# Optimization experiments

Measured on AMD Instinct MI355X. Metric: run time of the kernel, lower is better.

The kernel has to match this reference:

```python
import jax, jax.numpy as jnp
import numpy as np

KE_KCAL = 332.0636  # Coulomb constant, kcal/mol * Angstrom / e^2
R_CUT = 5.0
R_ON = R_CUT / 4.0
R_OFF = 3.0 * R_CUT / 4.0
B, A, F = 32, 1024, 128  # molecules, atoms per molecule, feature dim
MAX_Z = 86


def silu(x):
    return x * jax.nn.sigmoid(x)


def res_mlp(x, W1, W2, Wout):
    # Residual (two pre-activation linears) -> activation -> Linear, no biases
    h = silu(x) @ W1
    h = silu(h) @ W2
    return silu(x + h) @ Wout


def f_switch(r):
    # smooth switching function built from sigma(x)=exp(-1/x) for x>0 else 0
    arg = (r - R_ON) / (R_OFF - R_ON)
    def sigma(x):
        xs = jnp.where(x > 0, x, 1.0)
        return jnp.where(x > 0, jnp.exp(-1.0 / xs), 0.0)
    num = sigma(1.0 - arg)
    return num / (num + sigma(arg))


def setup_inputs() -> dict:
    key = jax.random.key(0)
    ks = jax.random.split(key, 16)
    box = 22.0  # ~liquid density box for 1024 atoms (Angstrom)
    s = 1.0 / np.sqrt(F)
    return {
        'e_z': jax.random.normal(ks[0], (B * A, F), jnp.float32) * 0.1,
        'charge': jax.random.normal(ks[1], (B,), jnp.float32),
        'xyz': jax.random.uniform(ks[2], (B, A, 3), jnp.float32) * box,
        'W_lin': jax.random.normal(ks[3], (F, F), jnp.float32) * s,
        'b_lin': jnp.zeros((F,), jnp.float32),
        'k_plus': jax.random.normal(ks[4], (F,), jnp.float32) * s,
        'k_minus': jax.random.normal(ks[5], (F,), jnp.float32) * s,
        'v_plus': jax.random.normal(ks[6], (F,), jnp.float32) * s,
        'v_minus': jax.random.normal(ks[7], (F,), jnp.float32) * s,
        'Wr1': jax.random.normal(ks[8], (F, F), jnp.float32) * s,
        'Wr2': jax.random.normal(ks[9], (F, F), jnp.float32) * s,
        'Wout': jax.random.normal(ks[10], (F, F), jnp.float32) * s,
        'w_e': jax.random.normal(ks[11], (F,), jnp.float32) * s,
        'q_z_table': jax.random.normal(ks[12], (MAX_Z,), jnp.float32) * 0.01,
        'z': jax.random.randint(ks[13], (B * A,), 1, MAX_Z, jnp.int32),
    }


def reference(e_z, charge, xyz, W_lin, b_lin, k_plus, k_minus, v_plus, v_minus,
              Wr1, Wr2, Wout, w_e, q_z_table, z):
    # ---- ElectronicEmbedding (per-molecule loop vectorized over B) ----
    q = (e_z @ W_lin + b_lin).reshape(B, A, F)
    pos = (charge >= 0)[:, None]                       # [B,1]
    k = jnp.where(pos, k_plus[None, :], k_minus[None, :])   # [B,F]
    v = jnp.where(pos, v_plus[None, :], v_minus[None, :])   # [B,F]
    arg = jnp.einsum('baf,bf->ba', q, k) / np.sqrt(F)
    num = jax.nn.softplus(arg)                         # log(1+exp)
    a = charge[:, None] * num / num.sum(axis=1, keepdims=True)  # [B,A]
    av = a[:, :, None] * v[:, None, :]                 # [B,A,F]
    e_psi = res_mlp(av.reshape(B * A, F), Wr1, Wr2, Wout)
    f = e_z + e_psi                                    # atom features [N,F]

    # ---- Electrostatics.get_charge (charge-conserving correction) ----
    pred_q = (f @ w_e + q_z_table[z]).reshape(B, A)
    corr = (charge - pred_q.sum(axis=1)) / A
    q_atom = pred_q + corr[:, None]                    # [B,A]

    # ---- Electrostatics.get_en: O(A^2) pairwise switched Coulomb ----
    diff = xyz[:, :, None, :] - xyz[:, None, :, :]     # [B,A,A,3]
    r2 = jnp.sum(diff * diff, axis=-1)                 # [B,A,A]
    mask = jnp.triu(jnp.ones((A, A), bool), k=1)       # pairs j > i (r>0)
    r = jnp.sqrt(jnp.where(mask, r2, 1.0))
    fs = f_switch(r)
    coul = fs / jnp.sqrt(r * r + 1.0) + (1.0 - fs) / r
    pair_e = q_atom[:, :, None] * q_atom[:, None, :] * coul
    energy = KE_KCAL * jnp.sum(jnp.where(mask, pair_e, 0.0), axis=(1, 2))  # [B]
    return energy
```

## Files before the change

### kernel.cpp

```cpp
#include <hip/hip_runtime.h>
#include <math.h>

#define B_MOL 32
#define A_AT  1024
#define NF    128
#define N_AT  (B_MOL * A_AT)

#define WS_K2P     0
#define WS_K2M     128
#define WS_WOUT    256
#define WS_C       384
#define WS_NUMSUM  512
#define WS_PREDSUM 544
#define WS_NUM     1024
#define WS_EZWE    (WS_NUM + N_AT)
#define WS_PRED    (WS_EZWE + N_AT)
#define WS_SIDX    (WS_PRED + N_AT)
#define WS_SPOS    (WS_SIDX + N_AT)
#define WS_W1F     (WS_SPOS + 4 * N_AT)
#define WS_W2F     (WS_W1F + 8192)

typedef short short8 __attribute__((ext_vector_type(8)));
typedef float floatx4 __attribute__((ext_vector_type(4)));

__device__ __forceinline__ float fast_rcp(float x) { return __builtin_amdgcn_rcpf(x); }
__device__ __forceinline__ float fast_rsq(float x) { return __builtin_amdgcn_rsqf(x); }
__device__ __forceinline__ float silu_f(float x) { return x * fast_rcp(1.f + __expf(-x)); }

__device__ __forceinline__ short f2bf(float x) {
  unsigned u = __float_as_uint(x);
  u += 0x7fffu + ((u >> 16) & 1u);
  return (short)(u >> 16);
}

__device__ __forceinline__ float wave_sum(float v) {
#pragma unroll
  for (int o = 32; o > 0; o >>= 1) v += __shfl_xor(v, o, 64);
  return v;
}

__global__ __launch_bounds__(256) void pre_kernel(const float* __restrict__ W_lin,
                                                  const float* __restrict__ b_lin,
                                                  const float* __restrict__ k_plus,
                                                  const float* __restrict__ k_minus,
                                                  const float* __restrict__ Wout,
                                                  const float* __restrict__ w_e,
                                                  const float* __restrict__ Wr1,
                                                  const float* __restrict__ Wr2,
                                                  float* __restrict__ ws,
                                                  float* __restrict__ out) {
  int tid = threadIdx.x;
  if (blockIdx.x < 2) {
    const float* W = (blockIdx.x == 0) ? Wr1 : Wr2;
    short* dst = (short*)(ws + ((blockIdx.x == 0) ? WS_W1F : WS_W2F));
#pragma unroll
    for (int it = 0; it < 8; it++) {
      int idx = it * 256 + tid;
      int fi = idx >> 6, lane = idx & 63;
      int nt = fi >> 2, ks = fi & 3;
      int q = lane >> 4, n15 = lane & 15;
      int k0 = ks * 32 + q * 8;
      int col = nt * 16 + n15;
#pragma unroll
      for (int j = 0; j < 8; j++)
        dst[fi * 512 + lane * 8 + j] = f2bf(W[(k0 + j) * NF + col]);
    }
  } else {
    if (tid < 128) {
      float sp = 0.f, sm = 0.f;
      for (int f = 0; f < NF; f++) {
        float wl = W_lin[tid * NF + f];
        sp = fmaf(wl, k_plus[f], sp);
        sm = fmaf(wl, k_minus[f], sm);
      }
      ws[WS_K2P + tid] = sp;
      ws[WS_K2M + tid] = sm;
      if (tid < 2) {
        const float* kk = (tid == 0) ? k_plus : k_minus;
        float c = 0.f;
        for (int f = 0; f < NF; f++) c = fmaf(b_lin[f], kk[f], c);
        ws[WS_C + tid] = c;
      }
    } else {
      int g = tid - 128;
      float sw = 0.f;
      for (int f = 0; f < NF; f++) sw = fmaf(Wout[g * NF + f], w_e[f], sw);
      ws[WS_WOUT + g] = sw;
      if (g < 64) ws[WS_NUMSUM + g] = 0.f;
      if (g < 32) out[g] = 0.f;
    }
  }
}

__global__ __launch_bounds__(256) void sort_kernel(const float* __restrict__ xyz,
                                                   float* __restrict__ ws) {
  int mol = blockIdx.x, tid = threadIdx.x;
  __shared__ int hist[64], start[64];
  if (tid < 64) hist[tid] = 0;
  __syncthreads();
  float px[4], py[4], pz[4];
  int cell[4];
#pragma unroll
  for (int r = 0; r < 4; r++) {
    int j = tid + r * 256;
    const float* p = xyz + (size_t)(mol * A_AT + j) * 3;
    px[r] = p[0]; py[r] = p[1]; pz[r] = p[2];
    int cx = min(3, max(0, (int)(px[r] * (4.f / 22.f))));
    int cy = min(3, max(0, (int)(py[r] * (4.f / 22.f))));
    int cz = min(3, max(0, (int)(pz[r] * (4.f / 22.f))));
    cell[r] = cx * 16 + cy * 4 + cz;
    atomicAdd(&hist[cell[r]], 1);
  }
  __syncthreads();
  if (tid == 0) {
    int s = 0;
    for (int c = 0; c < 64; c++) { start[c] = s; s += hist[c]; }
  }
  __syncthreads();
  float4* spos = (float4*)(ws + WS_SPOS);
  int* sidx = (int*)ws + WS_SIDX;
#pragma unroll
  for (int r = 0; r < 4; r++) {
    int j = tid + r * 256;
    int off = atomicAdd(&start[cell[r]], 1);
    int g = mol * A_AT + off;
    spos[g] = make_float4(px[r], py[r], pz[r], 0.f);
    sidx[g] = j;
  }
}

__global__ __launch_bounds__(256) void attn_kernel(const float* __restrict__ e_z,
                                                   const float* __restrict__ charge,
                                                   const float* __restrict__ w_e,
                                                   float* __restrict__ ws) {
  int tid = threadIdx.x;
  int t = blockIdx.x * 256 + tid;
  int n = t >> 2;
  int part = t & 3;
  int mol = blockIdx.x >> 4;
  __shared__ float k2[NF], wesh[NF];
  float ch = charge[mol];
  if (tid < 128) {
    const float* k2src = ws + (ch >= 0.f ? WS_K2P : WS_K2M);
    k2[tid] = k2src[tid];
    wesh[tid] = w_e[tid];
  }
  float cc = ws[WS_C + (ch >= 0.f ? 0 : 1)];
  __syncthreads();
  const float4* row = (const float4*)(e_z + (size_t)n * NF + part * 32);
  float dk = 0.f, dw = 0.f;
#pragma unroll 8
  for (int i = 0; i < 8; i++) {
    float4 v = row[i];
    int b = part * 32 + i * 4;
    dk = fmaf(v.x, k2[b+0], dk); dk = fmaf(v.y, k2[b+1], dk);
    dk = fmaf(v.z, k2[b+2], dk); dk = fmaf(v.w, k2[b+3], dk);
    dw = fmaf(v.x, wesh[b+0], dw); dw = fmaf(v.y, wesh[b+1], dw);
    dw = fmaf(v.z, wesh[b+2], dw); dw = fmaf(v.w, wesh[b+3], dw);
  }
  dk += __shfl_xor(dk, 1, 64); dk += __shfl_xor(dk, 2, 64);
  dw += __shfl_xor(dw, 1, 64); dw += __shfl_xor(dw, 2, 64);
  float num = 0.f;
  if (part == 0) {
    float arg = (dk + cc) * 0.08838834764831845f;
    num = fmaxf(arg, 0.f) + log1pf(__expf(-fabsf(arg)));
    ws[WS_NUM + n] = num;
    ws[WS_EZWE + n] = dw;
  }
  float s = wave_sum(num);
  if ((tid & 63) == 0) atomicAdd(&ws[WS_NUMSUM + mol], s);
}

__global__ __launch_bounds__(256) void mlp_kernel(const float* __restrict__ charge,
                                                  const float* __restrict__ v_plus,
                                                  const float* __restrict__ v_minus,
                                                  const int* __restrict__ z,
                                                  const float* __restrict__ qz_table,
                                                  float* __restrict__ ws) {
  int base = blockIdx.x * 64;
  int mol = base >> 10;
  int tid = threadIdx.x;
  int w = tid >> 6;
  int lane = tid & 63;
  int q = lane >> 4, l15 = lane & 15;

  __shared__ short wf[16384];
  __shared__ short a2s[4 * 16 * 136];
  __shared__ float vsh[NF], wout_sh[NF], awsh[64], pred_sh[64];

  float ch = charge[mol];
  if (tid < 128) {
    vsh[tid] = (ch >= 0.f) ? v_plus[tid] : v_minus[tid];
    wout_sh[tid] = ws[WS_WOUT + tid];
  }
  if (tid < 64) awsh[tid] = ch * ws[WS_NUM + base + tid] / ws[WS_NUMSUM + mol];

  {
    const float4* src = (const float4*)(ws + WS_W1F);
    float4* dst = (float4*)wf;
#pragma unroll
    for (int r = 0; r < 8; r++) dst[tid + r * 256] = src[tid + r * 256];
  }
  __syncthreads();

  float aw_m = awsh[w * 16 + l15];
  floatx4 acc1[8];
#pragma unroll
  for (int nt = 0; nt < 8; nt++) acc1[nt] = (floatx4)(0.f);

#pragma unroll
  for (int ks = 0; ks < 4; ks++) {
    float4 va = *(const float4*)&vsh[ks * 32 + q * 8];
    float4 vb = *(const float4*)&vsh[ks * 32 + q * 8 + 4];
    short8 af;
    af[0] = f2bf(silu_f(aw_m * va.x)); af[1] = f2bf(silu_f(aw_m * va.y));
    af[2] = f2bf(silu_f(aw_m * va.z)); af[3] = f2bf(silu_f(aw_m * va.w));
    af[4] = f2bf(silu_f(aw_m * vb.x)); af[5] = f2bf(silu_f(aw_m * vb.y));
    af[6] = f2bf(silu_f(aw_m * vb.z)); af[7] = f2bf(silu_f(aw_m * vb.w));
#pragma unroll
    for (int nt = 0; nt < 8; nt++) {
      short8 bf = *(const short8*)&wf[(nt * 4 + ks) * 512 + lane * 8];
      acc1[nt] = __builtin_amdgcn_mfma_f32_16x16x32_bf16(af, bf, acc1[nt], 0, 0, 0);
    }
  }

#pragma unroll
  for (int nt = 0; nt < 8; nt++) {
    int f = nt * 16 + l15;
#pragma unroll
    for (int r = 0; r < 4; r++)
      a2s[w * 2176 + (q * 4 + r) * 136 + f] = f2bf(silu_f(acc1[nt][r]));
  }
  __syncthreads();
  {
    const float4* src = (const float4*)(ws + WS_W2F);
    float4* dst = (float4*)wf;
#pragma unroll
    for (int r = 0; r < 8; r++) dst[tid + r * 256] = src[tid + r * 256];
  }
  __syncthreads();

  floatx4 acc2[8];
#pragma unroll
  for (int nt = 0; nt < 8; nt++) acc2[nt] = (floatx4)(0.f);

#pragma unroll
  for (int ks = 0; ks < 4; ks++) {
    short8 af = *(const short8*)&a2s[w * 2176 + l15 * 136 + ks * 32 + q * 8];
#pragma unroll
    for (int nt = 0; nt < 8; nt++) {
      short8 bf = *(const short8*)&wf[(nt * 4 + ks) * 512 + lane * 8];
      acc2[nt] = __builtin_amdgcn_mfma_f32_16x16x32_bf16(af, bf, acc2[nt], 0, 0, 0);
    }
  }

  float awq[4], part[4];
#pragma unroll
  for (int r = 0; r < 4; r++) {
    awq[r] = awsh[w * 16 + q * 4 + r];
    part[r] = 0.f;
  }
#pragma unroll
  for (int nt = 0; nt < 8; nt++) {
    int f = nt * 16 + l15;
    float vv = vsh[f], ww = wout_sh[f];
#pragma unroll
    for (int r = 0; r < 4; r++) {
      float s = silu_f(fmaf(awq[r], vv, acc2[nt][r]));
      part[r] = fmaf(s, ww, part[r]);
    }
  }
#pragma unroll
  for (int r = 0; r < 4; r++) {
#pragma unroll
    for (int o = 1; o < 16; o <<= 1) part[r] += __shfl_xor(part[r], o, 64);
  }
  if (l15 == 0) {
#pragma unroll
    for (int r = 0; r < 4; r++) {
      int m = w * 16 + q * 4 + r;
      int n = base + m;
      float pred = part[r] + ws[WS_EZWE + n] + qz_table[z[n]];
      ws[WS_PRED + n] = pred;
      pred_sh[m] = pred;
    }
  }
  __syncthreads();
  if (tid < 64) {
    float s = wave_sum(pred_sh[tid]);
    if (tid == 0) atomicAdd(&ws[WS_PREDSUM + mol], s);
  }
}

__global__ __launch_bounds__(512) void pair_kernel(const float* __restrict__ xyz,
                                                   const float* __restrict__ charge,
                                                   float* __restrict__ ws,
                                                   float* __restrict__ out) {
  int bx = blockIdx.x;
  int mol = bx >> 4;
  int sub = bx & 15;
  int tid = threadIdx.x;
  __shared__ float4 posq[1024];
  __shared__ float wred[8];
  const float4* spos = (const float4*)(ws + WS_SPOS);
  const int* sidx = (const int*)ws + WS_SIDX;
  float corr = (charge[mol] - ws[WS_PREDSUM + mol]) * (1.f / 1024.f);
  for (int j = tid; j < 1024; j += 512) {
    float4 p = spos[mol * 1024 + j];
    p.w = ws[WS_PRED + mol * 1024 + sidx[mol * 1024 + j]] + corr;
    posq[j] = p;
  }
  __syncthreads();
  int i = sub * 64 + (tid & 63);
  int jq = tid >> 6;
  float4 me = posq[i];
  float e = 0.f;
  int j0 = jq * 128;
#pragma unroll 2
  for (int j = j0; j < j0 + 128; j++) {
    float4 p = posq[j];
    float dx = me.x - p.x, dy = me.y - p.y, dz = me.z - p.z;
    float r2 = fmaf(dx, dx, fmaf(dy, dy, dz * dz));
    bool self = (j == i);
    if (self) r2 = 1.0e8f;
    float qj = self ? 0.f : p.w;
    float inv_r = fast_rsq(r2);
    e = fmaf(qj, inv_r, e);
    if (__any(r2 < 14.0625f)) {
      float r = r2 * inv_r;
      float arg = (r - 1.25f) * 0.4f;
      float argc = fminf(fmaxf(arg, 1e-6f), 1.f - 1e-6f);
      float t = fast_rcp(argc) - fast_rcp(1.f - argc);
      float fs = fast_rcp(1.f + __expf(-t));
      float delta = fs * (fast_rsq(r2 + 1.f) - inv_r);
      e = fmaf(qj, delta, e);
    }
  }
  e *= me.w;
  float s = wave_sum(e);
  if ((tid & 63) == 0) wred[tid >> 6] = s;
  __syncthreads();
  if (tid == 0) {
    float tot = 0.f;
#pragma unroll
    for (int k = 0; k < 8; k++) tot += wred[k];
    atomicAdd(&out[mol], 166.0318f * tot);
  }
}

extern "C" void kernel_launch(void* const* d_in, const int* in_sizes, int n_in,
                              void* d_out, int out_size, void* d_ws, size_t ws_size,
                              hipStream_t stream) {
  const float* e_z     = (const float*)d_in[0];
  const float* charge  = (const float*)d_in[1];
  const float* xyz     = (const float*)d_in[2];
  const float* W_lin   = (const float*)d_in[3];
  const float* b_lin   = (const float*)d_in[4];
  const float* k_plus  = (const float*)d_in[5];
  const float* k_minus = (const float*)d_in[6];
  const float* v_plus  = (const float*)d_in[7];
  const float* v_minus = (const float*)d_in[8];
  const float* Wr1     = (const float*)d_in[9];
  const float* Wr2     = (const float*)d_in[10];
  const float* Wout    = (const float*)d_in[11];
  const float* w_e     = (const float*)d_in[12];
  const float* qz      = (const float*)d_in[13];
  const int*   z       = (const int*)d_in[14];
  float* out = (float*)d_out;
  float* ws  = (float*)d_ws;

  pre_kernel<<<3, 256, 0, stream>>>(W_lin, b_lin, k_plus, k_minus, Wout, w_e,
                                    Wr1, Wr2, ws, out);
  sort_kernel<<<32, 256, 0, stream>>>(xyz, ws);
  attn_kernel<<<512, 256, 0, stream>>>(e_z, charge, w_e, ws);
  mlp_kernel<<<512, 256, 0, stream>>>(charge, v_plus, v_minus, z, qz, ws);
  pair_kernel<<<512, 512, 0, stream>>>(xyz, charge, ws, out);
}
```

Before: 159.0 us.

## Exploit pair symmetry, merge setup kernels, coalesce attention and weight repacking

The pair kernel now evaluates only the upper-triangular sorted block pairs (c >= s), with a masked diagonal block, and doubles the prefactor. This roughly halves the O(A^2) Coulomb work but leaves load imbalance across waves. The sort and preprocessing kernels are merged into one launch to save a kernel dispatch. The attention dot products are restructured so 32 lanes read one row in a coalesced way, and the bf16 weight repack now reads W with float4 loads.

```diff
diff --git a/kernel.cpp b/kernel.cpp
--- a/kernel.cpp
+++ b/kernel.cpp
@@ -39,31 +39,70 @@
   return v;
 }
 
-__global__ __launch_bounds__(256) void pre_kernel(const float* __restrict__ W_lin,
-                                                  const float* __restrict__ b_lin,
-                                                  const float* __restrict__ k_plus,
-                                                  const float* __restrict__ k_minus,
-                                                  const float* __restrict__ Wout,
-                                                  const float* __restrict__ w_e,
-                                                  const float* __restrict__ Wr1,
-                                                  const float* __restrict__ Wr2,
-                                                  float* __restrict__ ws,
-                                                  float* __restrict__ out) {
-  int tid = threadIdx.x;
-  if (blockIdx.x < 2) {
-    const float* W = (blockIdx.x == 0) ? Wr1 : Wr2;
-    short* dst = (short*)(ws + ((blockIdx.x == 0) ? WS_W1F : WS_W2F));
-#pragma unroll
-    for (int it = 0; it < 8; it++) {
+__global__ __launch_bounds__(256) void setup_kernel(const float* __restrict__ xyz,
+                                                    const float* __restrict__ W_lin,
+                                                    const float* __restrict__ b_lin,
+                                                    const float* __restrict__ k_plus,
+                                                    const float* __restrict__ k_minus,
+                                                    const float* __restrict__ Wout,
+                                                    const float* __restrict__ w_e,
+                                                    const float* __restrict__ Wr1,
+                                                    const float* __restrict__ Wr2,
+                                                    float* __restrict__ ws,
+                                                    float* __restrict__ out) {
+  int bx = blockIdx.x, tid = threadIdx.x;
+  if (bx < 32) {
+    int mol = bx;
+    __shared__ int hist[64], start[64];
+    if (tid < 64) hist[tid] = 0;
+    __syncthreads();
+    float px[4], py[4], pz[4];
+    int cell[4];
+#pragma unroll
+    for (int r = 0; r < 4; r++) {
+      int j = tid + r * 256;
+      const float* p = xyz + (size_t)(mol * A_AT + j) * 3;
+      px[r] = p[0]; py[r] = p[1]; pz[r] = p[2];
+      int cx = min(3, max(0, (int)(px[r] * (4.f / 22.f))));
+      int cy = min(3, max(0, (int)(py[r] * (4.f / 22.f))));
+      int cz = min(3, max(0, (int)(pz[r] * (4.f / 22.f))));
+      cell[r] = cx * 16 + cy * 4 + cz;
+      atomicAdd(&hist[cell[r]], 1);
+    }
+    __syncthreads();
+    if (tid == 0) {
+      int s = 0;
+      for (int c = 0; c < 64; c++) { start[c] = s; s += hist[c]; }
+    }
+    __syncthreads();
+    float4* spos = (float4*)(ws + WS_SPOS);
+    int* sidx = (int*)ws + WS_SIDX;
+#pragma unroll
+    for (int r = 0; r < 4; r++) {
+      int j = tid + r * 256;
+      int off = atomicAdd(&start[cell[r]], 1);
+      int g = mol * A_AT + off;
+      spos[g] = make_float4(px[r], py[r], pz[r], 0.f);
+      sidx[g] = j;
+    }
+  } else if (bx < 34) {
+    const float* W = (bx == 32) ? Wr1 : Wr2;
+    short* dst = (short*)(ws + ((bx == 32) ? WS_W1F : WS_W2F));
+#pragma unroll
+    for (int it = 0; it < 16; it++) {
       int idx = it * 256 + tid;
-      int fi = idx >> 6, lane = idx & 63;
-      int nt = fi >> 2, ks = fi & 3;
-      int q = lane >> 4, n15 = lane & 15;
-      int k0 = ks * 32 + q * 8;
-      int col = nt * 16 + n15;
-#pragma unroll
-      for (int j = 0; j < 8; j++)
-        dst[fi * 512 + lane * 8 + j] = f2bf(W[(k0 + j) * NF + col]);
+      int k = idx >> 5;
+      int c0 = (idx & 31) * 4;
+      float4 v = ((const float4*)W)[idx];
+      int ks = k >> 5, q = (k & 31) >> 3, j = k & 7;
+      float vv[4] = {v.x, v.y, v.z, v.w};
+#pragma unroll
+      for (int e = 0; e < 4; e++) {
+        int col = c0 + e;
+        int fi = (col >> 4) * 4 + ks;
+        int lane = q * 16 + (col & 15);
+        dst[fi * 512 + lane * 8 + j] = f2bf(vv[e]);
+      }
     }
   } else {
     if (tid < 128) {
@@ -92,53 +131,16 @@
   }
 }
 
-__global__ __launch_bounds__(256) void sort_kernel(const float* __restrict__ xyz,
-                                                   float* __restrict__ ws) {
-  int mol = blockIdx.x, tid = threadIdx.x;
-  __shared__ int hist[64], start[64];
-  if (tid < 64) hist[tid] = 0;
-  __syncthreads();
-  float px[4], py[4], pz[4];
-  int cell[4];
-#pragma unroll
-  for (int r = 0; r < 4; r++) {
-    int j = tid + r * 256;
-    const float* p = xyz + (size_t)(mol * A_AT + j) * 3;
-    px[r] = p[0]; py[r] = p[1]; pz[r] = p[2];
-    int cx = min(3, max(0, (int)(px[r] * (4.f / 22.f))));
-    int cy = min(3, max(0, (int)(py[r] * (4.f / 22.f))));
-    int cz = min(3, max(0, (int)(pz[r] * (4.f / 22.f))));
-    cell[r] = cx * 16 + cy * 4 + cz;
-    atomicAdd(&hist[cell[r]], 1);
-  }
-  __syncthreads();
-  if (tid == 0) {
-    int s = 0;
-    for (int c = 0; c < 64; c++) { start[c] = s; s += hist[c]; }
-  }
-  __syncthreads();
-  float4* spos = (float4*)(ws + WS_SPOS);
-  int* sidx = (int*)ws + WS_SIDX;
-#pragma unroll
-  for (int r = 0; r < 4; r++) {
-    int j = tid + r * 256;
-    int off = atomicAdd(&start[cell[r]], 1);
-    int g = mol * A_AT + off;
-    spos[g] = make_float4(px[r], py[r], pz[r], 0.f);
-    sidx[g] = j;
-  }
-}
-
 __global__ __launch_bounds__(256) void attn_kernel(const float* __restrict__ e_z,
                                                    const float* __restrict__ charge,
                                                    const float* __restrict__ w_e,
                                                    float* __restrict__ ws) {
+  int bx = blockIdx.x;
+  int mol = bx >> 4;
+  int base = bx * 64;
   int tid = threadIdx.x;
-  int t = blockIdx.x * 256 + tid;
-  int n = t >> 2;
-  int part = t & 3;
-  int mol = blockIdx.x >> 4;
-  __shared__ float k2[NF], wesh[NF];
+  int w = tid >> 6, l = tid & 63, half = l >> 5, l31 = l & 31;
+  __shared__ float k2[NF], wesh[NF], numred[4];
   float ch = charge[mol];
   if (tid < 128) {
     const float* k2src = ws + (ch >= 0.f ? WS_K2P : WS_K2M);
@@ -147,28 +149,35 @@
   }
   float cc = ws[WS_C + (ch >= 0.f ? 0 : 1)];
   __syncthreads();
-  const float4* row = (const float4*)(e_z + (size_t)n * NF + part * 32);
-  float dk = 0.f, dw = 0.f;
-#pragma unroll 8
-  for (int i = 0; i < 8; i++) {
-    float4 v = row[i];
-    int b = part * 32 + i * 4;
-    dk = fmaf(v.x, k2[b+0], dk); dk = fmaf(v.y, k2[b+1], dk);
-    dk = fmaf(v.z, k2[b+2], dk); dk = fmaf(v.w, k2[b+3], dk);
-    dw = fmaf(v.x, wesh[b+0], dw); dw = fmaf(v.y, wesh[b+1], dw);
-    dw = fmaf(v.z, wesh[b+2], dw); dw = fmaf(v.w, wesh[b+3], dw);
-  }
-  dk += __shfl_xor(dk, 1, 64); dk += __shfl_xor(dk, 2, 64);
-  dw += __shfl_xor(dw, 1, 64); dw += __shfl_xor(dw, 2, 64);
-  float num = 0.f;
-  if (part == 0) {
-    float arg = (dk + cc) * 0.08838834764831845f;
-    num = fmaxf(arg, 0.f) + log1pf(__expf(-fabsf(arg)));
-    ws[WS_NUM + n] = num;
-    ws[WS_EZWE + n] = dw;
-  }
-  float s = wave_sum(num);
-  if ((tid & 63) == 0) atomicAdd(&ws[WS_NUMSUM + mol], s);
+  int b = l31 * 4;
+  float k0 = k2[b], k1 = k2[b+1], k2v = k2[b+2], k3 = k2[b+3];
+  float w0 = wesh[b], w1 = wesh[b+1], w2 = wesh[b+2], w3 = wesh[b+3];
+  float wavenum = 0.f;
+#pragma unroll
+  for (int it = 0; it < 8; it++) {
+    int m = it * 8 + w * 2 + half;
+    int n = base + m;
+    float4 v = *((const float4*)(e_z + (size_t)n * NF) + l31);
+    float dk = v.x*k0; dk = fmaf(v.y, k1, dk); dk = fmaf(v.z, k2v, dk); dk = fmaf(v.w, k3, dk);
+    float dw = v.x*w0; dw = fmaf(v.y, w1, dw); dw = fmaf(v.z, w2, dw); dw = fmaf(v.w, w3, dw);
+#pragma unroll
+    for (int o = 1; o < 32; o <<= 1) {
+      dk += __shfl_xor(dk, o, 64);
+      dw += __shfl_xor(dw, o, 64);
+    }
+    if (l31 == 0) {
+      float arg = (dk + cc) * 0.08838834764831845f;
+      float num = fmaxf(arg, 0.f) + log1pf(__expf(-fabsf(arg)));
+      ws[WS_NUM + n] = num;
+      ws[WS_EZWE + n] = dw;
+      wavenum += num;
+    }
+  }
+  wavenum += __shfl_xor(wavenum, 32, 64);
+  if (l == 0) numred[w] = wavenum;
+  __syncthreads();
+  if (tid == 0)
+    atomicAdd(&ws[WS_NUMSUM + mol], numred[0] + numred[1] + numred[2] + numred[3]);
 }
 
 __global__ __launch_bounds__(256) void mlp_kernel(const float* __restrict__ charge,
@@ -292,60 +301,78 @@
   }
 }
 
-__global__ __launch_bounds__(512) void pair_kernel(const float* __restrict__ xyz,
-                                                   const float* __restrict__ charge,
+__global__ __launch_bounds__(256) void pair_kernel(const float* __restrict__ charge,
                                                    float* __restrict__ ws,
                                                    float* __restrict__ out) {
   int bx = blockIdx.x;
   int mol = bx >> 4;
-  int sub = bx & 15;
+  int s = bx & 15;
   int tid = threadIdx.x;
+  int w = tid >> 6, lane = tid & 63;
   __shared__ float4 posq[1024];
-  __shared__ float wred[8];
+  __shared__ float wred[4];
   const float4* spos = (const float4*)(ws + WS_SPOS);
   const int* sidx = (const int*)ws + WS_SIDX;
   float corr = (charge[mol] - ws[WS_PREDSUM + mol]) * (1.f / 1024.f);
-  for (int j = tid; j < 1024; j += 512) {
+  for (int j = tid; j < 1024; j += 256) {
     float4 p = spos[mol * 1024 + j];
     p.w = ws[WS_PRED + mol * 1024 + sidx[mol * 1024 + j]] + corr;
     posq[j] = p;
   }
   __syncthreads();
-  int i = sub * 64 + (tid & 63);
-  int jq = tid >> 6;
+  int i = s * 64 + lane;
   float4 me = posq[i];
   float e = 0.f;
-  int j0 = jq * 128;
-#pragma unroll 2
-  for (int j = j0; j < j0 + 128; j++) {
-    float4 p = posq[j];
-    float dx = me.x - p.x, dy = me.y - p.y, dz = me.z - p.z;
-    float r2 = fmaf(dx, dx, fmaf(dy, dy, dz * dz));
-    bool self = (j == i);
-    if (self) r2 = 1.0e8f;
-    float qj = self ? 0.f : p.w;
-    float inv_r = fast_rsq(r2);
-    e = fmaf(qj, inv_r, e);
-    if (__any(r2 < 14.0625f)) {
-      float r = r2 * inv_r;
-      float arg = (r - 1.25f) * 0.4f;
-      float argc = fminf(fmaxf(arg, 1e-6f), 1.f - 1e-6f);
-      float t = fast_rcp(argc) - fast_rcp(1.f - argc);
-      float fs = fast_rcp(1.f + __expf(-t));
-      float delta = fs * (fast_rsq(r2 + 1.f) - inv_r);
-      e = fmaf(qj, delta, e);
+  for (int c = s + w; c < 16; c += 4) {
+    int j0 = c * 64;
+    if (c == s) {
+#pragma unroll 4
+      for (int j = j0; j < j0 + 64; j++) {
+        float4 p = posq[j];
+        float dx = me.x - p.x, dy = me.y - p.y, dz = me.z - p.z;
+        float r2 = fmaf(dx, dx, fmaf(dy, dy, dz * dz));
+        bool skip = (j <= i);
+        float r2s = skip ? 1.0e8f : r2;
+        float qj = skip ? 0.f : p.w;
+        float inv_r = fast_rsq(r2s);
+        e = fmaf(qj, inv_r, e);
+        if (__any(r2s < 14.0625f)) {
+          float r = r2s * inv_r;
+          float arg = (r - 1.25f) * 0.4f;
+          float argc = fminf(fmaxf(arg, 1e-6f), 1.f - 1e-6f);
+          float t = fast_rcp(argc) - fast_rcp(1.f - argc);
+          float fs = fast_rcp(1.f + __expf(-t));
+          float delta = fs * (fast_rsq(r2s + 1.f) - inv_r);
+          e = fmaf(qj, delta, e);
+        }
+      }
+    } else {
+#pragma unroll 4
+      for (int j = j0; j < j0 + 64; j++) {
+        float4 p = posq[j];
+        float dx = me.x - p.x, dy = me.y - p.y, dz = me.z - p.z;
+        float r2 = fmaf(dx, dx, fmaf(dy, dy, dz * dz));
+        float qj = p.w;
+        float inv_r = fast_rsq(r2);
+        e = fmaf(qj, inv_r, e);
+        if (__any(r2 < 14.0625f)) {
+          float r = r2 * inv_r;
+          float arg = (r - 1.25f) * 0.4f;
+          float argc = fminf(fmaxf(arg, 1e-6f), 1.f - 1e-6f);
+          float t = fast_rcp(argc) - fast_rcp(1.f - argc);
+          float fs = fast_rcp(1.f + __expf(-t));
+          float delta = fs * (fast_rsq(r2 + 1.f) - inv_r);
+          e = fmaf(qj, delta, e);
+        }
+      }
     }
   }
   e *= me.w;
-  float s = wave_sum(e);
-  if ((tid & 63) == 0) wred[tid >> 6] = s;
-  __syncthreads();
-  if (tid == 0) {
-    float tot = 0.f;
-#pragma unroll
-    for (int k = 0; k < 8; k++) tot += wred[k];
-    atomicAdd(&out[mol], 166.0318f * tot);
-  }
+  float sred = wave_sum(e);
+  if (lane == 0) wred[w] = sred;
+  __syncthreads();
+  if (tid == 0)
+    atomicAdd(&out[mol], 332.0636f * (wred[0] + wred[1] + wred[2] + wred[3]));
 }
 
 extern "C" void kernel_launch(void* const* d_in, const int* in_sizes, int n_in,
@@ -369,10 +396,9 @@
   float* out = (float*)d_out;
   float* ws  = (float*)d_ws;
 
-  pre_kernel<<<3, 256, 0, stream>>>(W_lin, b_lin, k_plus, k_minus, Wout, w_e,
-                                    Wr1, Wr2, ws, out);
-  sort_kernel<<<32, 256, 0, stream>>>(xyz, ws);
+  setup_kernel<<<35, 256, 0, stream>>>(xyz, W_lin, b_lin, k_plus, k_minus,
+                                       Wout, w_e, Wr1, Wr2, ws, out);
   attn_kernel<<<512, 256, 0, stream>>>(e_z, charge, w_e, ws);
   mlp_kernel<<<512, 256, 0, stream>>>(charge, v_plus, v_minus, z, qz, ws);
-  pair_kernel<<<512, 512, 0, stream>>>(xyz, charge, ws, out);
-}
+  pair_kernel<<<512, 256, 0, stream>>>(charge, ws, out);
+}
```

Result: faster. 147.9 us (-7.0%).
